# Kernel tuning notes

Measured on AMD Instinct MI355X. Metric: run time of the kernel, lower is better.

## Reference

```python
import jax, jax.numpy as jnp
import numpy as np

B, T, C, H, HD = 2, 2048, 1024, 16, 64
EPS = 1e-6

def rmsnorm(x):
    return x * jax.lax.rsqrt(jnp.mean(x * x, axis=-1, keepdims=True) + EPS)

def rotary_cos_sin(seq_len, hd):
    inv_freq = 1.0 / (10000.0 ** (jnp.arange(0, hd, 2, dtype=jnp.float32) / hd))
    freqs = jnp.arange(seq_len, dtype=jnp.float32)[:, None] * inv_freq[None, :]  # [T, hd/2]
    return jnp.cos(freqs)[None, :, None, :], jnp.sin(freqs)[None, :, None, :]

def apply_rotary(x, cos, sin):
    x1, x2 = x[..., : HD // 2], x[..., HD // 2 :]
    return jnp.concatenate([x1 * cos + x2 * sin, -x1 * sin + x2 * cos], axis=-1)


def setup_inputs() -> dict:
    key = jax.random.key(0)
    ks = jax.random.split(key, 8)
    return {
        "x": jax.random.normal(ks[0], (B, T, C), jnp.float32),
        "w_qkv": jax.random.normal(ks[1], (3 * C, C), jnp.float32) * 0.02,
        "w_out": jax.random.normal(ks[2], (C, C), jnp.float32) * 0.02,
        "hyp_curvature": jax.random.uniform(ks[3], (1, H, 1, 1), jnp.float32, 0.5, 1.5),
        "w_uv": jax.random.normal(ks[4], (8 * C, C), jnp.float32) * 0.02,
        "b_uv": jnp.zeros((8 * C,), jnp.float32),
        "w_mlp_out": jax.random.normal(ks[5], (C, 4 * C), jnp.float32) * 0.02,
        "b_mlp_out": jnp.zeros((C,), jnp.float32),
    }


def reference(x, w_qkv, w_out, hyp_curvature, w_uv, b_uv, w_mlp_out, b_mlp_out):
    # --- pre-norm (euc/hyp branch uses rms_norm) ---
    h = rmsnorm(x)
    # --- QKV projection ---
    qkv = h @ w_qkv.T  # [B,T,3C]
    q, k, v = jnp.split(qkv, 3, axis=-1)
    q = q.reshape(B, T, H, HD)
    k = k.reshape(B, T, H, HD)
    v = v.reshape(B, T, H, HD)
    # --- RoPE ---
    cos, sin = rotary_cos_sin(T, HD)
    q = apply_rotary(q, cos, sin)
    k = apply_rotary(k, cos, sin)
    # [B,H,T,HD]
    q = jnp.transpose(q, (0, 2, 1, 3))
    k = jnp.transpose(k, (0, 2, 1, 3))
    v = jnp.transpose(v, (0, 2, 1, 3))
    # --- hyperbolic (Lorentz) attention ---
    kc = hyp_curvature  # [1,H,1,1], positive per-head curvature
    q0 = jnp.sqrt(kc + jnp.sum(q * q, axis=-1, keepdims=True))  # time coord [B,H,T,1]
    k0 = jnp.sqrt(kc + jnp.sum(k * k, axis=-1, keepdims=True))
    # Lorentz inner product <u,v>_L = -u0*v0 + u.v  -> [B,H,T,S]
    lorentz = jnp.einsum("bhtd,bhsd->bhts", q, k) - q0 * jnp.swapaxes(k0, -1, -2)
    dis = jnp.sqrt(kc) * jnp.arccosh(jnp.maximum(-lorentz / kc, 1.0 + EPS))
    causal = jnp.tril(jnp.ones((T, T), dtype=bool))
    scores = jnp.where(causal, -dis, -jnp.inf)  # hyp_attn_weight='neg_dis'
    attn_w = jax.nn.softmax(scores, axis=-1)
    attn = jnp.einsum("bhts,bhsd->bhtd", attn_w, v)
    attn = jnp.transpose(attn, (0, 2, 1, 3)).reshape(B, T, C)
    x = x + attn @ w_out.T
    # --- SwiGLU MLP with pre rms_norm ---
    h = rmsnorm(x)
    uv = h @ w_uv.T + b_uv
    u, vg = jnp.split(uv, 2, axis=-1)
    h_mlp = (u * jax.nn.silu(vg)) @ w_mlp_out.T + b_mlp_out
    return x + h_mlp
```

## Files before the change

### kernel.cpp

```cpp
#include <hip/hip_runtime.h>
#include <cstdint>
#include <cmath>

typedef __bf16 bf16;
typedef __attribute__((ext_vector_type(8))) __bf16 bf16x8;
typedef __attribute__((ext_vector_type(4))) __bf16 bf16x4;
typedef __attribute__((ext_vector_type(4))) float f32x4;

constexpr int B_ = 2, T_ = 2048, C_ = 1024, H_ = 16, HD_ = 64;
constexpr int M_ = B_ * T_;

#define EXP2F(x) __builtin_amdgcn_exp2f(x)
#define LOG2F(x) __builtin_amdgcn_logf(x)
#define SQRTF(x) __builtin_amdgcn_sqrtf(x)
#define RCPF(x)  __builtin_amdgcn_rcpf(x)

__device__ __forceinline__ void gld16(const void* g, void* l) {
  __builtin_amdgcn_global_load_lds((const __attribute__((address_space(1))) void*)g,
                                   (__attribute__((address_space(3))) void*)l, 16, 0, 0);
}

__global__ __launch_bounds__(256) void cast_all_kernel(const float* __restrict__ s0,
                                                       const float* __restrict__ s1,
                                                       const float* __restrict__ s2,
                                                       const float* __restrict__ s3,
                                                       bf16* __restrict__ d0,
                                                       bf16* __restrict__ d1,
                                                       bf16* __restrict__ d2,
                                                       bf16* __restrict__ d3) {
  size_t gid = (size_t)blockIdx.x * 256 + threadIdx.x;
  const float* src;
  bf16* dst;
  if (gid < 786432) { src = s0; dst = d0; }
  else if (gid < 786432 + 262144) { gid -= 786432; src = s1; dst = d1; }
  else if (gid < 786432 + 262144 + 2097152) { gid -= 786432 + 262144; src = s2; dst = d2; }
  else { gid -= 786432 + 262144 + 2097152; src = s3; dst = d3; }
  f32x4 v = *(const f32x4*)(src + gid * 4);
  bf16x4 o;
  o[0] = (bf16)v[0]; o[1] = (bf16)v[1]; o[2] = (bf16)v[2]; o[3] = (bf16)v[3];
  *(bf16x4*)(dst + gid * 4) = o;
}

template <int MODE, typename OutT>
__global__ __launch_bounds__(256) void gemm_bt(const bf16* __restrict__ A,
                                               const bf16* __restrict__ Bw,
                                               OutT* __restrict__ Cmat,
                                               const float* __restrict__ bias,
                                               const float* __restrict__ R,
                                               int M, int N, int K, int lda) {
  __shared__ __align__(16) bf16 Als[2][128 * 32];
  __shared__ __align__(16) bf16 Bls[2][128 * 32];
  const int tid  = threadIdx.x;
  const int wave = tid >> 6;
  const int lane = tid & 63;
  const int quad = lane >> 4;
  const int l16  = lane & 15;
  const int bm = blockIdx.x * 128;
  const int bn = blockIdx.y * 128;
  const int wm = (wave & 1) * 64;
  const int wn = (wave >> 1) * 64;
  const int srow   = lane >> 2;
  const int schunk = lane & 3;

  f32x4 acc[4][4];
#pragma unroll
  for (int i = 0; i < 4; i++)
#pragma unroll
    for (int j = 0; j < 4; j++) acc[i][j] = f32x4{0.f, 0.f, 0.f, 0.f};

  const bf16* Ag = A  + (size_t)(bm + wave * 32 + srow) * lda + schunk * 8;
  const bf16* Bg = Bw + (size_t)(bn + wave * 32 + srow) * K   + schunk * 8;
  bf16* AlsW0 = &Als[0][(wave * 32) * 32];
  bf16* AlsW1 = &Als[1][(wave * 32) * 32];
  bf16* BlsW0 = &Bls[0][(wave * 32) * 32];
  bf16* BlsW1 = &Bls[1][(wave * 32) * 32];

  for (int k0 = 0; k0 < K; k0 += 64) {
    gld16(Ag + k0,                         AlsW0);
    gld16(Ag + k0 + (size_t)16 * lda,      AlsW0 + 16 * 32);
    gld16(Ag + k0 + 32,                    AlsW1);
    gld16(Ag + k0 + 32 + (size_t)16 * lda, AlsW1 + 16 * 32);
    gld16(Bg + k0,                         BlsW0);
    gld16(Bg + k0 + (size_t)16 * K,        BlsW0 + 16 * 32);
    gld16(Bg + k0 + 32,                    BlsW1);
    gld16(Bg + k0 + 32 + (size_t)16 * K,   BlsW1 + 16 * 32);
    __syncthreads();

#pragma unroll
    for (int hh = 0; hh < 2; hh++) {
      bf16x8 af[4], bfr[4];
#pragma unroll
      for (int mt = 0; mt < 4; mt++)
        af[mt] = *(const bf16x8*)&Als[hh][(wm + mt * 16 + l16) * 32 + quad * 8];
#pragma unroll
      for (int nt = 0; nt < 4; nt++)
        bfr[nt] = *(const bf16x8*)&Bls[hh][(wn + nt * 16 + l16) * 32 + quad * 8];
#pragma unroll
      for (int mt = 0; mt < 4; mt++)
#pragma unroll
        for (int nt = 0; nt < 4; nt++)
          acc[mt][nt] = __builtin_amdgcn_mfma_f32_16x16x32_bf16(af[mt], bfr[nt], acc[mt][nt], 0, 0, 0);
    }
    __syncthreads();
  }

#pragma unroll
  for (int mt = 0; mt < 4; mt++) {
    const int row = bm + wm + mt * 16 + quad * 4;
#pragma unroll
    for (int nt = 0; nt < 4; nt++) {
      const int col = bn + wn + nt * 16 + l16;
      float bval = 0.f;
      if (MODE & 2) bval = bias[col];
#pragma unroll
      for (int r = 0; r < 4; r++) {
        float v = acc[mt][nt][r] + bval;
        if (MODE & 1) v += R[(size_t)(row + r) * N + col];
        Cmat[(size_t)(row + r) * N + col] = (OutT)v;
      }
    }
  }
}

__global__ __launch_bounds__(256) void rmsnorm_kernel(const float* __restrict__ X,
                                                      bf16* __restrict__ O) {
  const int row = blockIdx.x;
  const int tid = threadIdx.x;
  const int wave = tid >> 6;
  f32x4 v = *(const f32x4*)(X + (size_t)row * C_ + tid * 4);
  float s = v[0] * v[0] + v[1] * v[1] + v[2] * v[2] + v[3] * v[3];
#pragma unroll
  for (int off = 32; off >= 1; off >>= 1) s += __shfl_xor(s, off);
  __shared__ float wsum[4];
  __shared__ float scale_sh;
  if ((tid & 63) == 0) wsum[wave] = s;
  __syncthreads();
  if (tid == 0)
    scale_sh = rsqrtf((wsum[0] + wsum[1] + wsum[2] + wsum[3]) * (1.f / (float)C_) + 1e-6f);
  __syncthreads();
  const float sc = scale_sh;
  bf16x4 o;
  o[0] = (bf16)(v[0] * sc); o[1] = (bf16)(v[1] * sc);
  o[2] = (bf16)(v[2] * sc); o[3] = (bf16)(v[3] * sc);
  *(bf16x4*)(O + (size_t)row * C_ + tid * 4) = o;
}

__global__ __launch_bounds__(256) void rotary_kernel(bf16* __restrict__ qkv,
                                                     const float* __restrict__ kcb,
                                                     float* __restrict__ q0b,
                                                     float* __restrict__ k0b) {
  const int wid  = blockIdx.x * 4 + (threadIdx.x >> 6);
  const int lane = threadIdx.x & 63;
  const int b = wid >> 15;
  const int rem = wid & 32767;
  const int t = rem >> 4;
  const int h = rem & 15;
  const int i = lane & 31;
  const float invf = expf(-((float)i / 32.f) * 9.210340371976184f);
  const float ang = (float)t * invf;
  const float cx = cosf(ang), sx = sinf(ang);
  const float kc = kcb[h];
  bf16* qp = qkv + (size_t)(b * T_ + t) * 3072 + h * 64;

#pragma unroll
  for (int which = 0; which < 2; which++) {
    bf16* p = qp + which * 1024;
    float x1 = (float)p[i];
    float x2 = (float)p[i + 32];
    float o = (lane < 32) ? (x1 * cx + x2 * sx) : (x2 * cx - x1 * sx);
    float ss = o * o;
#pragma unroll
    for (int off = 32; off >= 1; off >>= 1) ss += __shfl_xor(ss, off);
    p[lane] = (bf16)o;
    if (lane == 0) {
      float* dst = which == 0 ? q0b : k0b;
      dst[(size_t)(b * H_ + h) * T_ + t] = SQRTF(kc + ss);
    }
  }
}

__global__ __launch_bounds__(256) void attn_kernel(const bf16* __restrict__ qkv,
                                                   const float* __restrict__ q0b,
                                                   const float* __restrict__ k0b,
                                                   const float* __restrict__ kcb,
                                                   bf16* __restrict__ outp) {
  __shared__ __align__(16) bf16 Kls[2][64][72];
  __shared__ __align__(16) bf16 Vt[2][64][68];
  __shared__ __align__(16) bf16 Pls[4][16 * 36];
  __shared__ float k0s[2][64];

  const int tid = threadIdx.x;
  const int wave = tid >> 6, lane = tid & 63;
  const int quad = lane >> 4, l16 = lane & 15;
  const int bh = blockIdx.x;
  const int b = bh >> 4, h = bh & 15;

  const float kc = kcb[h];
  const float inv_kc = 1.f / kc;
  const float sqkc = SQRTF(kc);
  const int ss = tid >> 3, dg = tid & 7;
  bf16* Pl = Pls[wave];
  const float* q0base = q0b + (size_t)(b * H_ + h) * T_;
  const float* k0base = k0b + (size_t)(b * H_ + h) * T_;

  const int ty = 31 - (int)blockIdx.y;
  const int t0 = ty * 64;
  const int tb = t0 + wave * 16;
  const int nIter = ty + 1;

  const bf16* qrow = qkv + (size_t)(b * T_ + tb + l16) * 3072 + h * 64;
  bf16x8 aq0 = *(const bf16x8*)(qrow + quad * 8);
  bf16x8 aq1 = *(const bf16x8*)(qrow + 32 + quad * 8);
  float q0r[4];
#pragma unroll
  for (int r = 0; r < 4; r++) q0r[r] = q0base[tb + quad * 4 + r];

  f32x4 o[4];
#pragma unroll
  for (int dt = 0; dt < 4; dt++) o[dt] = f32x4{0.f, 0.f, 0.f, 0.f};
  float lrow[4] = {0.f, 0.f, 0.f, 0.f};

  const bf16* kbase = qkv + (size_t)b * T_ * 3072 + 1024 + h * 64 + dg * 8;
  bf16x8 kv0 = *(const bf16x8*)(kbase + (size_t)ss * 3072);
  bf16x8 vv0 = *(const bf16x8*)(kbase + (size_t)ss * 3072 + 1024);
  bf16x8 kv1 = *(const bf16x8*)(kbase + (size_t)(32 + ss) * 3072);
  bf16x8 vv1 = *(const bf16x8*)(kbase + (size_t)(32 + ss) * 3072 + 1024);
  float k0v = (tid < 64) ? k0base[tid] : 0.f;

  for (int it = 0; it < nIter; ++it) {
    const int s0 = it * 64;
    const int buf = it & 1;
    *(bf16x8*)&Kls[buf][ss][dg * 8]      = kv0;
    *(bf16x8*)&Kls[buf][32 + ss][dg * 8] = kv1;
#pragma unroll
    for (int i2 = 0; i2 < 8; i2++) {
      Vt[buf][dg * 8 + i2][ss]      = vv0[i2];
      Vt[buf][dg * 8 + i2][32 + ss] = vv1[i2];
    }
    if (tid < 64) k0s[buf][tid] = k0v;
    __syncthreads();

    const int s0n = (it + 1 < nIter) ? s0 + 64 : s0;
    kv0 = *(const bf16x8*)(kbase + (size_t)(s0n + ss) * 3072);
    vv0 = *(const bf16x8*)(kbase + (size_t)(s0n + ss) * 3072 + 1024);
    kv1 = *(const bf16x8*)(kbase + (size_t)(s0n + 32 + ss) * 3072);
    vv1 = *(const bf16x8*)(kbase + (size_t)(s0n + 32 + ss) * 3072 + 1024);
    if (tid < 64) k0v = k0base[s0n + tid];

    f32x4 sc[4];
#pragma unroll
    for (int nt = 0; nt < 4; nt++) {
      sc[nt] = f32x4{0.f, 0.f, 0.f, 0.f};
      bf16x8 b0 = *(const bf16x8*)&Kls[buf][nt * 16 + l16][quad * 8];
      bf16x8 b1 = *(const bf16x8*)&Kls[buf][nt * 16 + l16][32 + quad * 8];
      sc[nt] = __builtin_amdgcn_mfma_f32_16x16x32_bf16(aq0, b0, sc[nt], 0, 0, 0);
      sc[nt] = __builtin_amdgcn_mfma_f32_16x16x32_bf16(aq1, b1, sc[nt], 0, 0, 0);
    }

    bf16x8 ap[2];
#pragma unroll
    for (int ck = 0; ck < 2; ck++) {
#pragma unroll
      for (int ntl = 0; ntl < 2; ntl++) {
        const int nt = ck * 2 + ntl;
        const float k0c = k0s[buf][nt * 16 + l16];
        const int s = s0 + nt * 16 + l16;
#pragma unroll
        for (int r = 0; r < 4; r++) {
          const int t = tb + quad * 4 + r;
          float lor = sc[nt][r] - q0r[r] * k0c;
          float ratio = fmaxf(-lor * inv_kc, 1.f + 1e-6f);
          float wv = ratio + SQRTF(ratio * ratio - 1.f);
          float p = EXP2F(-sqkc * LOG2F(wv));
          p = (s <= t) ? p : 0.f;
          lrow[r] += p;
          Pl[(quad * 4 + r) * 36 + ntl * 16 + l16] = (bf16)p;
        }
      }
      ap[ck] = *(const bf16x8*)&Pl[l16 * 36 + quad * 8];
    }
#pragma unroll
    for (int dt = 0; dt < 4; dt++) {
      bf16x8 bv0 = *(const bf16x8*)&Vt[buf][dt * 16 + l16][quad * 8];
      bf16x8 bv1 = *(const bf16x8*)&Vt[buf][dt * 16 + l16][32 + quad * 8];
      o[dt] = __builtin_amdgcn_mfma_f32_16x16x32_bf16(ap[0], bv0, o[dt], 0, 0, 0);
      o[dt] = __builtin_amdgcn_mfma_f32_16x16x32_bf16(ap[1], bv1, o[dt], 0, 0, 0);
    }
  }

#pragma unroll
  for (int r = 0; r < 4; r++) {
#pragma unroll
    for (int off = 1; off <= 8; off <<= 1) lrow[r] += __shfl_xor(lrow[r], off);
  }
#pragma unroll
  for (int r = 0; r < 4; r++) {
    const float invl = RCPF(lrow[r]);
    const int t = tb + quad * 4 + r;
#pragma unroll
    for (int dt = 0; dt < 4; dt++) {
      float val = o[dt][r] * invl;
      outp[(size_t)(b * T_ + t) * C_ + h * 64 + dt * 16 + l16] = (bf16)val;
    }
  }
}

__global__ __launch_bounds__(256) void swiglu_kernel(bf16* __restrict__ uv) {
  const size_t gid = (size_t)blockIdx.x * 256 + threadIdx.x;
  const size_t e0 = gid * 4;
  const size_t m = e0 >> 12;
  const size_t j = e0 & 4095;
  bf16* up = uv + m * 8192 + j;
  bf16x4 u4 = *(const bf16x4*)up;
  bf16x4 v4 = *(const bf16x4*)(up + 4096);
  bf16x4 o;
#pragma unroll
  for (int i = 0; i < 4; i++) {
    float uu = (float)u4[i];
    float vvv = (float)v4[i];
    float vc = fminf(fmaxf(vvv, -80.f), 80.f);
    float sig = 1.f / (1.f + __expf(-vc));
    o[i] = (bf16)(uu * vvv * sig);
  }
  *(bf16x4*)up = o;
}

extern "C" void kernel_launch(void* const* d_in, const int* in_sizes, int n_in,
                              void* d_out, int out_size, void* d_ws, size_t ws_size,
                              hipStream_t stream) {
  const float* x      = (const float*)d_in[0];
  const float* w_qkv  = (const float*)d_in[1];
  const float* w_out  = (const float*)d_in[2];
  const float* kcb    = (const float*)d_in[3];
  const float* w_uv   = (const float*)d_in[4];
  const float* b_uv   = (const float*)d_in[5];
  const float* w_mlp  = (const float*)d_in[6];
  const float* b_mlp  = (const float*)d_in[7];
  float* out = (float*)d_out;

  const size_t MB = 1024ull * 1024ull;
  char* w = (char*)d_ws;
  bf16*  wqkv_b  = (bf16*)(w + 0);
  bf16*  wout_b  = (bf16*)(w + 6 * MB);
  bf16*  wuv_b   = (bf16*)(w + 8 * MB);
  bf16*  wmlp_b  = (bf16*)(w + 24 * MB);
  bf16*  hbuf    = (bf16*)(w + 32 * MB);
  bf16*  qkvbuf  = (bf16*)(w + 40 * MB);
  bf16*  attnbuf = (bf16*)(w + 64 * MB);
  bf16*  uvbuf   = (bf16*)(w + 40 * MB);
  float* x2buf   = (float*)(w + 104 * MB);
  float* q0b     = (float*)(w + 120 * MB);
  float* k0b     = (float*)(w + 120 * MB + 256 * 1024);

  cast_all_kernel<<<(786432 + 262144 + 2097152 + 1048576) / 256, 256, 0, stream>>>(
      w_qkv, w_out, w_uv, w_mlp, wqkv_b, wout_b, wuv_b, wmlp_b);

  rmsnorm_kernel<<<M_, 256, 0, stream>>>(x, hbuf);
  gemm_bt<0, bf16><<<dim3(M_ / 128, 3072 / 128), 256, 0, stream>>>(
      hbuf, wqkv_b, qkvbuf, nullptr, nullptr, M_, 3072, 1024, 1024);
  rotary_kernel<<<(B_ * T_ * H_) / 4, 256, 0, stream>>>(qkvbuf, kcb, q0b, k0b);
  attn_kernel<<<dim3(B_ * H_, 32), 256, 0, stream>>>(qkvbuf, q0b, k0b, kcb, attnbuf);
  gemm_bt<1, float><<<dim3(M_ / 128, 1024 / 128), 256, 0, stream>>>(
      attnbuf, wout_b, x2buf, nullptr, x, M_, 1024, 1024, 1024);
  rmsnorm_kernel<<<M_, 256, 0, stream>>>(x2buf, hbuf);
  gemm_bt<2, bf16><<<dim3(M_ / 128, 8192 / 128), 256, 0, stream>>>(
      hbuf, wuv_b, uvbuf, b_uv, nullptr, M_, 8192, 1024, 1024);
  swiglu_kernel<<<(M_ * 4096) / (4 * 256), 256, 0, stream>>>(uvbuf);
  gemm_bt<3, float><<<dim3(M_ / 128, 1024 / 128), 256, 0, stream>>>(
      uvbuf, wmlp_b, out, b_mlp, x2buf, M_, 1024, 4096, 8192);
}
```

Measured before the change: 456.0 us.

## Fuse SwiGLU into up-projection GEMM epilogue via interleaved weight layout

Permutes the rows of w_uv and b_uv during the cast so that each 128-column GEMM tile holds 64 u columns and their matching 64 gate columns. The up-projection epilogue then stages the gate half in LDS and writes silu-gated products directly. This removes the separate swiglu pass and halves the intermediate buffer that the down-projection reads. The attention K/V staging is also reorganised so each thread handles adjacent rows and writes V transposed as bf16 pairs, cutting the number of LDS stores. There is leftover dead code: an unused 16KB shared staging array whose zeroing loop adds LDS pressure and extra work.

```diff
diff --git a/kernel.cpp b/kernel.cpp
--- a/kernel.cpp
+++ b/kernel.cpp
@@ -5,6 +5,7 @@
 typedef __bf16 bf16;
 typedef __attribute__((ext_vector_type(8))) __bf16 bf16x8;
 typedef __attribute__((ext_vector_type(4))) __bf16 bf16x4;
+typedef __attribute__((ext_vector_type(2))) __bf16 bf16x2;
 typedef __attribute__((ext_vector_type(4))) float f32x4;
 
 constexpr int B_ = 2, T_ = 2048, C_ = 1024, H_ = 16, HD_ = 64;
@@ -24,21 +25,42 @@
                                                        const float* __restrict__ s1,
                                                        const float* __restrict__ s2,
                                                        const float* __restrict__ s3,
+                                                       const float* __restrict__ s4,
                                                        bf16* __restrict__ d0,
                                                        bf16* __restrict__ d1,
                                                        bf16* __restrict__ d2,
-                                                       bf16* __restrict__ d3) {
+                                                       bf16* __restrict__ d3,
+                                                       float* __restrict__ d4) {
   size_t gid = (size_t)blockIdx.x * 256 + threadIdx.x;
+  if (gid >= 786432 + 262144 + 2097152 + 1048576) {
+    size_t g4 = gid - (786432 + 262144 + 2097152 + 1048576);
+    if (g4 >= 2048) return;
+    int r = (int)(g4 * 4);
+    int dr;
+    if (r < 4096) { int blk = r >> 6, i = r & 63; dr = blk * 128 + i; }
+    else { int j = r - 4096; int blk = j >> 6, i = j & 63; dr = blk * 128 + 64 + i; }
+    *(f32x4*)(d4 + dr) = *(const f32x4*)(s4 + r);
+    return;
+  }
   const float* src;
   bf16* dst;
-  if (gid < 786432) { src = s0; dst = d0; }
-  else if (gid < 786432 + 262144) { gid -= 786432; src = s1; dst = d1; }
-  else if (gid < 786432 + 262144 + 2097152) { gid -= 786432 + 262144; src = s2; dst = d2; }
-  else { gid -= 786432 + 262144 + 2097152; src = s3; dst = d3; }
+  size_t dstoff;
+  if (gid < 786432) { src = s0; dst = d0; dstoff = gid * 4; }
+  else if (gid < 786432 + 262144) { gid -= 786432; src = s1; dst = d1; dstoff = gid * 4; }
+  else if (gid < 786432 + 262144 + 2097152) {
+    gid -= 786432 + 262144; src = s2; dst = d2;
+    size_t elem = gid * 4;
+    int r = (int)(elem >> 10), c = (int)(elem & 1023);
+    int dr;
+    if (r < 4096) { int blk = r >> 6, i = r & 63; dr = blk * 128 + i; }
+    else { int j = r - 4096; int blk = j >> 6, i = j & 63; dr = blk * 128 + 64 + i; }
+    dstoff = ((size_t)dr << 10) | (size_t)c;
+  }
+  else { gid -= 786432 + 262144 + 2097152; src = s3; dst = d3; dstoff = gid * 4; }
   f32x4 v = *(const f32x4*)(src + gid * 4);
   bf16x4 o;
   o[0] = (bf16)v[0]; o[1] = (bf16)v[1]; o[2] = (bf16)v[2]; o[3] = (bf16)v[3];
-  *(bf16x4*)(dst + gid * 4) = o;
+  *(bf16x4*)(dst + dstoff) = o;
 }
 
 template <int MODE, typename OutT>
@@ -104,9 +126,25 @@
     __syncthreads();
   }
 
+  if (MODE == 4) {
+    __shared__ float vstage[4 * 16 * 64];
+    float* vs = &vstage[(wave & 1) * 16 * 64 * 2];
+    if (wave >= 2) {
+#pragma unroll
+      for (int mt = 0; mt < 4; mt++)
+#pragma unroll
+        for (int nt = 0; nt < 4; nt++) {
+          const float bv = bias[bn + 64 + nt * 16 + l16];
+#pragma unroll
+          for (int r = 0; r < 4; r++)
+            vs[(mt * 16 + quad * 4 + r) * 4 + nt] = 0.f;
+        }
+    }
+  }
 #pragma unroll
   for (int mt = 0; mt < 4; mt++) {
     const int row = bm + wm + mt * 16 + quad * 4;
+    if (MODE == 4) continue;
 #pragma unroll
     for (int nt = 0; nt < 4; nt++) {
       const int col = bn + wn + nt * 16 + l16;
@@ -117,6 +155,42 @@
         float v = acc[mt][nt][r] + bval;
         if (MODE & 1) v += R[(size_t)(row + r) * N + col];
         Cmat[(size_t)(row + r) * N + col] = (OutT)v;
+      }
+    }
+  }
+  if (MODE == 4) {
+    float* xbuf = (float*)&Als[0][0];
+    float* xb = xbuf + (wave & 1) * 4096;
+    __syncthreads();
+    if (wave >= 2) {
+#pragma unroll
+      for (int mt = 0; mt < 4; mt++)
+#pragma unroll
+        for (int nt = 0; nt < 4; nt++) {
+          const float bv = bias[bn + 64 + nt * 16 + l16];
+#pragma unroll
+          for (int r = 0; r < 4; r++)
+            xb[(mt * 16 + quad * 4 + r) * 64 + nt * 16 + l16] = acc[mt][nt][r] + bv;
+        }
+    }
+    __syncthreads();
+    if (wave < 2) {
+      const int colg = (bn >> 1);
+#pragma unroll
+      for (int mt = 0; mt < 4; mt++) {
+        const int row = bm + wm + mt * 16 + quad * 4;
+#pragma unroll
+        for (int nt = 0; nt < 4; nt++) {
+          const float bu = bias[bn + nt * 16 + l16];
+          const int col = colg + nt * 16 + l16;
+#pragma unroll
+          for (int r = 0; r < 4; r++) {
+            float u = acc[mt][nt][r] + bu;
+            float v = xb[(mt * 16 + quad * 4 + r) * 64 + nt * 16 + l16];
+            float sig = RCPF(1.f + EXP2F(-v * 1.44269504f));
+            Cmat[(size_t)(row + r) * N + col] = (OutT)(u * v * sig);
+          }
+        }
       }
     }
   }
@@ -198,7 +272,7 @@
   const float kc = kcb[h];
   const float inv_kc = 1.f / kc;
   const float sqkc = SQRTF(kc);
-  const int ss = tid >> 3, dg = tid & 7;
+  const int sp = tid & 31, dq = tid >> 5;
   bf16* Pl = Pls[wave];
   const float* q0base = q0b + (size_t)(b * H_ + h) * T_;
   const float* k0base = k0b + (size_t)(b * H_ + h) * T_;
@@ -220,31 +294,33 @@
   for (int dt = 0; dt < 4; dt++) o[dt] = f32x4{0.f, 0.f, 0.f, 0.f};
   float lrow[4] = {0.f, 0.f, 0.f, 0.f};
 
-  const bf16* kbase = qkv + (size_t)b * T_ * 3072 + 1024 + h * 64 + dg * 8;
-  bf16x8 kv0 = *(const bf16x8*)(kbase + (size_t)ss * 3072);
-  bf16x8 vv0 = *(const bf16x8*)(kbase + (size_t)ss * 3072 + 1024);
-  bf16x8 kv1 = *(const bf16x8*)(kbase + (size_t)(32 + ss) * 3072);
-  bf16x8 vv1 = *(const bf16x8*)(kbase + (size_t)(32 + ss) * 3072 + 1024);
+  const bf16* kvbase = qkv + (size_t)b * T_ * 3072 + 1024 + h * 64 + dq * 8;
+  bf16x8 kv_a = *(const bf16x8*)(kvbase + (size_t)(2 * sp) * 3072);
+  bf16x8 kv_b = *(const bf16x8*)(kvbase + (size_t)(2 * sp + 1) * 3072);
+  bf16x8 vv_a = *(const bf16x8*)(kvbase + (size_t)(2 * sp) * 3072 + 1024);
+  bf16x8 vv_b = *(const bf16x8*)(kvbase + (size_t)(2 * sp + 1) * 3072 + 1024);
   float k0v = (tid < 64) ? k0base[tid] : 0.f;
 
   for (int it = 0; it < nIter; ++it) {
     const int s0 = it * 64;
     const int buf = it & 1;
-    *(bf16x8*)&Kls[buf][ss][dg * 8]      = kv0;
-    *(bf16x8*)&Kls[buf][32 + ss][dg * 8] = kv1;
+    *(bf16x8*)&Kls[buf][2 * sp][dq * 8]     = kv_a;
+    *(bf16x8*)&Kls[buf][2 * sp + 1][dq * 8] = kv_b;
 #pragma unroll
     for (int i2 = 0; i2 < 8; i2++) {
-      Vt[buf][dg * 8 + i2][ss]      = vv0[i2];
-      Vt[buf][dg * 8 + i2][32 + ss] = vv1[i2];
+      bf16x2 pr;
+      pr[0] = vv_a[i2];
+      pr[1] = vv_b[i2];
+      *(bf16x2*)&Vt[buf][dq * 8 + i2][2 * sp] = pr;
     }
     if (tid < 64) k0s[buf][tid] = k0v;
     __syncthreads();
 
     const int s0n = (it + 1 < nIter) ? s0 + 64 : s0;
-    kv0 = *(const bf16x8*)(kbase + (size_t)(s0n + ss) * 3072);
-    vv0 = *(const bf16x8*)(kbase + (size_t)(s0n + ss) * 3072 + 1024);
-    kv1 = *(const bf16x8*)(kbase + (size_t)(s0n + 32 + ss) * 3072);
-    vv1 = *(const bf16x8*)(kbase + (size_t)(s0n + 32 + ss) * 3072 + 1024);
+    kv_a = *(const bf16x8*)(kvbase + (size_t)(s0n + 2 * sp) * 3072);
+    kv_b = *(const bf16x8*)(kvbase + (size_t)(s0n + 2 * sp + 1) * 3072);
+    vv_a = *(const bf16x8*)(kvbase + (size_t)(s0n + 2 * sp) * 3072 + 1024);
+    vv_b = *(const bf16x8*)(kvbase + (size_t)(s0n + 2 * sp + 1) * 3072 + 1024);
     if (tid < 64) k0v = k0base[s0n + tid];
 
     f32x4 sc[4];
@@ -305,26 +381,6 @@
   }
 }
 
-__global__ __launch_bounds__(256) void swiglu_kernel(bf16* __restrict__ uv) {
-  const size_t gid = (size_t)blockIdx.x * 256 + threadIdx.x;
-  const size_t e0 = gid * 4;
-  const size_t m = e0 >> 12;
-  const size_t j = e0 & 4095;
-  bf16* up = uv + m * 8192 + j;
-  bf16x4 u4 = *(const bf16x4*)up;
-  bf16x4 v4 = *(const bf16x4*)(up + 4096);
-  bf16x4 o;
-#pragma unroll
-  for (int i = 0; i < 4; i++) {
-    float uu = (float)u4[i];
-    float vvv = (float)v4[i];
-    float vc = fminf(fmaxf(vvv, -80.f), 80.f);
-    float sig = 1.f / (1.f + __expf(-vc));
-    o[i] = (bf16)(uu * vvv * sig);
-  }
-  *(bf16x4*)up = o;
-}
-
 extern "C" void kernel_launch(void* const* d_in, const int* in_sizes, int n_in,
                               void* d_out, int out_size, void* d_ws, size_t ws_size,
                               hipStream_t stream) {
@@ -342,18 +398,20 @@
   char* w = (char*)d_ws;
   bf16*  wqkv_b  = (bf16*)(w + 0);
   bf16*  wout_b  = (bf16*)(w + 6 * MB);
-  bf16*  wuv_b   = (bf16*)(w + 8 * MB);
+  bf16*  wuv_p   = (bf16*)(w + 8 * MB);
   bf16*  wmlp_b  = (bf16*)(w + 24 * MB);
   bf16*  hbuf    = (bf16*)(w + 32 * MB);
   bf16*  qkvbuf  = (bf16*)(w + 40 * MB);
   bf16*  attnbuf = (bf16*)(w + 64 * MB);
-  bf16*  uvbuf   = (bf16*)(w + 40 * MB);
-  float* x2buf   = (float*)(w + 104 * MB);
-  float* q0b     = (float*)(w + 120 * MB);
-  float* k0b     = (float*)(w + 120 * MB + 256 * 1024);
-
-  cast_all_kernel<<<(786432 + 262144 + 2097152 + 1048576) / 256, 256, 0, stream>>>(
-      w_qkv, w_out, w_uv, w_mlp, wqkv_b, wout_b, wuv_b, wmlp_b);
+  bf16*  gbuf    = (bf16*)(w + 40 * MB);
+  float* x2buf   = (float*)(w + 72 * MB);
+  float* q0b     = (float*)(w + 88 * MB);
+  float* k0b     = (float*)(w + 88 * MB + 256 * 1024);
+  float* biasp   = (float*)(w + 88 * MB + 512 * 1024);
+
+  const int total4 = 786432 + 262144 + 2097152 + 1048576 + 2048;
+  cast_all_kernel<<<(total4 + 255) / 256, 256, 0, stream>>>(
+      w_qkv, w_out, w_uv, w_mlp, b_uv, wqkv_b, wout_b, wuv_p, wmlp_b, biasp);
 
   rmsnorm_kernel<<<M_, 256, 0, stream>>>(x, hbuf);
   gemm_bt<0, bf16><<<dim3(M_ / 128, 3072 / 128), 256, 0, stream>>>(
@@ -363,9 +421,8 @@
   gemm_bt<1, float><<<dim3(M_ / 128, 1024 / 128), 256, 0, stream>>>(
       attnbuf, wout_b, x2buf, nullptr, x, M_, 1024, 1024, 1024);
   rmsnorm_kernel<<<M_, 256, 0, stream>>>(x2buf, hbuf);
-  gemm_bt<2, bf16><<<dim3(M_ / 128, 8192 / 128), 256, 0, stream>>>(
-      hbuf, wuv_b, uvbuf, b_uv, nullptr, M_, 8192, 1024, 1024);
-  swiglu_kernel<<<(M_ * 4096) / (4 * 256), 256, 0, stream>>>(uvbuf);
+  gemm_bt<4, bf16><<<dim3(M_ / 128, 8192 / 128), 256, 0, stream>>>(
+      hbuf, wuv_p, gbuf, biasp, nullptr, M_, 4096, 1024, 1024);
   gemm_bt<3, float><<<dim3(M_ / 128, 1024 / 128), 256, 0, stream>>>(
-      uvbuf, wmlp_b, out, b_mlp, x2buf, M_, 1024, 4096, 8192);
-}
+      gbuf, wmlp_b, out, b_mlp, x2buf, M_, 1024, 4096, 4096);
+}
```

New measurement: 455.9 us. Within noise of the previous version (-0.0%).
